# Kernel optimization log

Hardware: AMD Instinct MI355X
Metric: run time of the kernel (lower is better)

The kernel has to match this reference:

```python
import jax, jax.numpy as jnp
import numpy as np

MODEL_DIMS = 2048
BATCH, SEQ = 4, 4096
NFREQ = MODEL_DIMS // 2 + 1  # rfft spectrum length


def setup_inputs() -> dict:
    key = jax.random.key(0)
    k1, k2, k3, k4 = jax.random.split(key, 4)
    x = jax.random.normal(k1, (BATCH, SEQ, MODEL_DIMS), dtype=jnp.float32)
    queries = jax.random.normal(k2, (1, 1, NFREQ), dtype=jnp.float32)
    keyvalues = jax.random.normal(k3, (1, 1, NFREQ), dtype=jnp.float32)
    # torch nn.Linear(model_dims, model_dims, bias=False): weight is [out, in]
    w_out = jax.random.normal(k4, (MODEL_DIMS, MODEL_DIMS), dtype=jnp.float32) * (MODEL_DIMS ** -0.5)
    return {"x": x, "queries": queries, "keyvalues": keyvalues, "w_out": w_out}


def reference(x, queries, keyvalues, w_out):
    # hrr.fft = rfft over feature dim -> complex64 [B, S, NFREQ]
    xhat = jnp.fft.rfft(x, axis=-1)
    q = xhat * queries            # real spectral params broadcast-multiply
    kv = xhat * keyvalues
    kv = jnp.cumsum(kv, axis=1)   # causal prefix sum over sequence
    qv = q * kv
    values_hat = jnp.fft.irfft(qv, n=x.shape[-1], axis=-1)  # back to real [B, S, D]
    # torch Linear: y = x @ W^T
    return jnp.einsum('bsd,ed->bse', values_hat, w_out)
```

## Files before the change

kernel.cpp:

```cpp
#include <hip/hip_runtime.h>
#include <hip/hip_bf16.h>
#include <stdint.h>

#define BATCH 4
#define SEQ   4096
#define DIM   2048
#define NFREQ 1025
#define NCPLX 1024
#define ROWS  (BATCH*SEQ)

#define SCH  16
#define NSC  (SEQ/SCH)
#define NSCG 16
#define NGRP (NSC/NSCG)

#define SPEC_STRIDE 257

typedef __bf16 bf16x8 __attribute__((ext_vector_type(8)));
typedef float  f32x4  __attribute__((ext_vector_type(4)));

__device__ __forceinline__ int drev4(int n) {
  return ((n&3)<<8) | (((n>>2)&3)<<6) | (((n>>4)&3)<<4) | (((n>>6)&3)<<2) | ((n>>8)&3);
}
#define ZI(i) ((i) + ((i)>>4))

__device__ __forceinline__ float2 cmulf(float2 a, float2 b) {
  return make_float2(a.x*b.x - a.y*b.y, a.x*b.y + a.y*b.x);
}

__device__ __forceinline__ unsigned short f2bf(float f) {
  union { float f; unsigned u; } v; v.f = f;
  unsigned r = v.u + 0x7fffu + ((v.u >> 16) & 1u);
  return (unsigned short)(r >> 16);
}
__device__ __forceinline__ unsigned packbf(float2 v) {
  return (unsigned)f2bf(v.x) | ((unsigned)f2bf(v.y) << 16);
}
__device__ __forceinline__ float2 unpackbf(unsigned u) {
  union { unsigned u; float f; } a, b;
  a.u = u << 16; b.u = u & 0xffff0000u;
  return make_float2(a.f, b.f);
}

template<int INV>
__device__ __forceinline__ void bfly4(float2* z, int i0, int q,
                                      float2 w1, float2 w2, float2 w3) {
  float2 x0 = z[ZI(i0)];
  float2 x1 = cmulf(z[ZI(i0+q)],   w1);
  float2 x2 = cmulf(z[ZI(i0+2*q)], w2);
  float2 x3 = cmulf(z[ZI(i0+3*q)], w3);
  float2 a = make_float2(x0.x+x2.x, x0.y+x2.y), b = make_float2(x0.x-x2.x, x0.y-x2.y);
  float2 c = make_float2(x1.x+x3.x, x1.y+x3.y), d = make_float2(x1.x-x3.x, x1.y-x3.y);
  z[ZI(i0)]     = make_float2(a.x+c.x, a.y+c.y);
  z[ZI(i0+2*q)] = make_float2(a.x-c.x, a.y-c.y);
  if (!INV) { z[ZI(i0+q)]   = make_float2(b.x+d.y, b.y-d.x);
              z[ZI(i0+3*q)] = make_float2(b.x-d.y, b.y+d.x); }
  else      { z[ZI(i0+q)]   = make_float2(b.x-d.y, b.y+d.x);
              z[ZI(i0+3*q)] = make_float2(b.x+d.y, b.y-d.x); }
}
template<int INV>
__device__ __forceinline__ void bfly4_nw(float2* z, int i0) {
  float2 x0=z[ZI(i0)], x1=z[ZI(i0+1)], x2=z[ZI(i0+2)], x3=z[ZI(i0+3)];
  float2 a = make_float2(x0.x+x2.x, x0.y+x2.y), b = make_float2(x0.x-x2.x, x0.y-x2.y);
  float2 c = make_float2(x1.x+x3.x, x1.y+x3.y), d = make_float2(x1.x-x3.x, x1.y-x3.y);
  z[ZI(i0)]   = make_float2(a.x+c.x, a.y+c.y);
  z[ZI(i0+2)] = make_float2(a.x-c.x, a.y-c.y);
  if (!INV) { z[ZI(i0+1)] = make_float2(b.x+d.y, b.y-d.x);
              z[ZI(i0+3)] = make_float2(b.x-d.y, b.y+d.x); }
  else      { z[ZI(i0+1)] = make_float2(b.x-d.y, b.y+d.x);
              z[ZI(i0+3)] = make_float2(b.x+d.y, b.y-d.x); }
}

template<int INV>
__device__ __forceinline__ void fft_stages_tw2(float2* z0, float2* z1, int tid,
                                               const float2* tw1) {
  { int b4 = tid*4;
    bfly4_nw<INV>(z0, b4);
    bfly4_nw<INV>(z1, b4);
  }
  __syncthreads();
#pragma unroll
  for (int s = 0; s < 4; ++s) {
    const int lq = 2 + 2*s;
    const int q  = 1 << lq;
    int j = tid & (q-1), g = tid >> lq;
    int base = (g << (lq+2)) + j;
    float2 w1 = tw1[s]; if (INV) w1.y = -w1.y;
    float2 w2 = cmulf(w1, w1), w3 = cmulf(w2, w1);
    bfly4<INV>(z0, base, q, w1, w2, w3);
    bfly4<INV>(z1, base, q, w1, w2, w3);
    __syncthreads();
  }
}

__device__ __forceinline__ void make_tw1(int tid, float2* tw1) {
#pragma unroll
  for (int s = 0; s < 4; ++s) {
    const int lq = 2 + 2*s;
    const int q  = 1 << lq;
    int j = tid & (q-1);
    float ang = -6.2831853071795864769f * (float)j / (float)(4*q);
    float sw, cw; __sincosf(ang, &sw, &cw);
    tw1[s] = make_float2(cw, sw);
  }
}

__device__ __forceinline__ void unpack_row(const float2* z, int tid,
    float cwA, float swA, float cwB, float swB,
    float2& vA, float2& vAp, float2& vB, float2& vBp) {
  float2 ZkA = z[ZI(tid)],     ZnA = z[ZI((NCPLX - tid) & (NCPLX-1))];
  float2 ZkB = z[ZI(tid+256)], ZnB = z[ZI(768 - tid)];
  float Er = 0.5f*(ZkA.x + ZnA.x), Ei = 0.5f*(ZkA.y - ZnA.y);
  float dr = 0.5f*(ZkA.x - ZnA.x), di = 0.5f*(ZkA.y + ZnA.y);
  vA  = make_float2( Er + cwA*di + swA*dr,  Ei + swA*di - cwA*dr);
  vAp = make_float2( Er - cwA*di - swA*dr, -Ei + swA*di - cwA*dr);
  float Fr = 0.5f*(ZkB.x + ZnB.x), Fi = 0.5f*(ZkB.y - ZnB.y);
  float er = 0.5f*(ZkB.x - ZnB.x), ei = 0.5f*(ZkB.y + ZnB.y);
  vB  = make_float2( Fr + cwB*ei + swB*er,  Fi + swB*ei - cwB*er);
  vBp = make_float2( Fr - cwB*ei - swB*er, -Fi + swB*ei - cwB*er);
}

__global__ __launch_bounds__(256) void fwd_wfft(const float* __restrict__ x,
                                                const float* __restrict__ w,
                                                const float* __restrict__ kvs,
                                                uint4* __restrict__ spec,
                                                float2* __restrict__ partial,
                                                unsigned short* __restrict__ H) {
  __shared__ float2 z0[ZI(1023)+2], z1[ZI(1023)+2];
  __shared__ __align__(16) unsigned short hrow[2][2048];
  const int tid = threadIdx.x;

  float2 tw1[4];
  make_tw1(tid, tw1);
  const int kA = tid, kB = tid + 256;
  float swA, cwA, swB, cwB;
  __sincosf(-3.14159265358979323846f * (float)kA / 1024.0f, &swA, &cwA);
  __sincosf(-3.14159265358979323846f * (float)kB / 1024.0f, &swB, &cwB);
  int id0 = ZI(drev4(2*tid)),     id1 = ZI(drev4(2*tid+1));
  int id2 = ZI(drev4(2*tid+512)), id3 = ZI(drev4(2*tid+513));

  if (blockIdx.x >= BATCH*NSC) {
    const int e0 = (blockIdx.x - BATCH*NSC) * 2;
    const float* wr0 = w + (size_t)e0 * DIM;
    const float* wr1 = wr0 + DIM;
    float4 a0 = ((const float4*)wr0)[tid], a1 = ((const float4*)wr0)[tid + 256];
    float4 b0 = ((const float4*)wr1)[tid], b1 = ((const float4*)wr1)[tid + 256];
    z0[id0] = make_float2(a0.x, a0.y); z0[id1] = make_float2(a0.z, a0.w);
    z0[id2] = make_float2(a1.x, a1.y); z0[id3] = make_float2(a1.z, a1.w);
    z1[id0] = make_float2(b0.x, b0.y); z1[id1] = make_float2(b0.z, b0.w);
    z1[id2] = make_float2(b1.x, b1.y); z1[id3] = make_float2(b1.z, b1.w);
    __syncthreads();
    fft_stages_tw2<0>(z0, z1, tid, tw1);
    const float invN = 1.0f/2048.0f, twoN = 2.0f/2048.0f;
    float aA = (tid == 0) ? invN : twoN;
#pragma unroll
    for (int r = 0; r < 2; ++r) {
      const float2* z = r ? z1 : z0;
      float2 vA, vAp, vB, vBp;
      unpack_row(z, tid, cwA, swA, cwB, swB, vA, vAp, vB, vBp);
      unsigned short* hr = hrow[r];
      hr[tid]        = f2bf(aA   * vA.x);
      hr[1024 - tid] = f2bf(aA   * vAp.x);
      hr[256 + tid]  = f2bf(twoN * vB.x);
      hr[768 - tid]  = f2bf(twoN * vBp.x);
      if (tid) {
        hr[1024 + tid] = f2bf(twoN * vA.y);
        hr[2048 - tid] = f2bf(twoN * vAp.y);
      }
      hr[1280 + tid] = f2bf(twoN * vB.y);
      hr[1792 - tid] = f2bf(twoN * vBp.y);
      if (tid == 0) {
        float2 Z5 = z[ZI(512)];
        hr[512]  = f2bf(twoN * Z5.x);
        hr[1536] = f2bf(twoN * (-Z5.y));
      }
    }
    __syncthreads();
    ((uint4*)(H + (size_t)e0 * DIM))[tid]       = ((const uint4*)hrow[0])[tid];
    ((uint4*)(H + (size_t)(e0 + 1) * DIM))[tid] = ((const uint4*)hrow[1])[tid];
    return;
  }

  const int sc = blockIdx.x & (NSC-1), b = blockIdx.x >> 8;
  float2 sA={0,0}, sAp={0,0}, sB={0,0}, sBp={0,0}, s5={0,0};
  const size_t row0 = (size_t)b*SEQ + (size_t)sc*SCH;
  const float* xrow = x + row0*DIM;
  const float kvA = kvs[kA], kvAp = kvs[NCPLX - kA], kvB = kvs[kB], kvBp = kvs[768 - tid];

  for (int s = 0; s < SCH; s += 2) {
    const float* xr0 = xrow + (size_t)s*DIM;
    const float* xr1 = xr0 + DIM;
    float4 a0 = ((const float4*)xr0)[tid], a1 = ((const float4*)xr0)[tid + 256];
    float4 b0 = ((const float4*)xr1)[tid], b1 = ((const float4*)xr1)[tid + 256];
    z0[id0] = make_float2(a0.x, a0.y); z0[id1] = make_float2(a0.z, a0.w);
    z0[id2] = make_float2(a1.x, a1.y); z0[id3] = make_float2(a1.z, a1.w);
    z1[id0] = make_float2(b0.x, b0.y); z1[id1] = make_float2(b0.z, b0.w);
    z1[id2] = make_float2(b1.x, b1.y); z1[id3] = make_float2(b1.z, b1.w);
    __syncthreads();
    fft_stages_tw2<0>(z0, z1, tid, tw1);
#pragma unroll
    for (int r = 0; r < 2; ++r) {
      const float2* z = r ? z1 : z0;
      float2 vA, vAp, vB, vBp;
      unpack_row(z, tid, cwA, swA, cwB, swB, vA, vAp, vB, vBp);
      sA.x += vA.x;  sA.y += vA.y;   sAp.x += vAp.x; sAp.y += vAp.y;
      sB.x += vB.x;  sB.y += vB.y;   sBp.x += vBp.x; sBp.y += vBp.y;
      uint4* sprow = spec + (row0 + s + r) * SPEC_STRIDE;
      sprow[tid] = make_uint4(packbf(vA), packbf(vAp), packbf(vB), packbf(vBp));
      if (tid == 0) {
        float2 Z5 = z[ZI(512)];
        float2 v5 = make_float2(Z5.x, -Z5.y);
        s5.x += v5.x; s5.y += v5.y;
        ((unsigned*)(sprow + 256))[0] = packbf(v5);
      }
    }
    __syncthreads();
  }
  float2* pp = partial + ((size_t)(b*NSC + sc)) * NFREQ;
  pp[kA]          = make_float2(kvA*sA.x,  kvA*sA.y);
  pp[NCPLX - kA]  = make_float2(kvAp*sAp.x, kvAp*sAp.y);
  pp[kB]          = make_float2(kvB*sB.x,  kvB*sB.y);
  pp[768 - tid]   = make_float2(kvBp*sBp.x, kvBp*sBp.y);
  if (tid == 0) { float kv5 = kvs[512]; pp[512] = make_float2(kv5*s5.x, kv5*s5.y); }
}

__global__ __launch_bounds__(256) void scanA(float2* __restrict__ partial,
                                             float2* __restrict__ gtot) {
  int kc = blockIdx.x % 5, g = (blockIdx.x / 5) % NGRP, b = blockIdx.x / (5*NGRP);
  int k = kc*256 + threadIdx.x;
  if (k >= NFREQ) return;
  float2* p = partial + ((size_t)(b*NSC + g*NSCG)) * NFREQ + k;
  float2 run = {0.f, 0.f};
#pragma unroll
  for (int i = 0; i < NSCG; ++i) {
    float2 t = p[(size_t)i*NFREQ];
    p[(size_t)i*NFREQ] = run;
    run.x += t.x; run.y += t.y;
  }
  gtot[((size_t)(b*NGRP + g)) * NFREQ + k] = run;
}

__global__ __launch_bounds__(256) void inv_fused(const uint4* __restrict__ spec,
                                                 const float* __restrict__ kvs,
                                                 const float* __restrict__ qs_,
                                                 const float2* __restrict__ partial,
                                                 const float2* __restrict__ gtot,
                                                 unsigned short* __restrict__ G) {
  __shared__ __align__(16) unsigned short grow[2][2048];
  const int tid = threadIdx.x;
  const int sc = blockIdx.x & (NSC-1), b = blockIdx.x >> 8;
  const int kA = tid, kB = tid + 256;

  float ksA = kvs[kA], ksAp = kvs[NCPLX - kA], ksB = kvs[kB], ksBp = kvs[768 - tid];
  float qsA = qs_[kA], qsAp = qs_[NCPLX - kA], qsB = qs_[kB], qsBp = qs_[768 - tid];

  const float2* pp = partial + ((size_t)(b*NSC + sc)) * NFREQ;
  float2 CA  = pp[kA], CAp = pp[NCPLX-kA], CB = pp[kB], CBp = pp[768-tid];
  float ks5 = kvs[512], qs5 = qs_[512];
  float2 C5 = pp[512];
  {
    const int g = sc >> 4;
    const float2* gb = gtot + (size_t)b*NGRP*NFREQ;
    for (int gg = 0; gg < g; ++gg) {
      const float2* gr = gb + (size_t)gg*NFREQ;
      float2 a0 = gr[kA], a1 = gr[NCPLX-kA], a2 = gr[kB], a3 = gr[768-tid];
      CA.x += a0.x; CA.y += a0.y;   CAp.x += a1.x; CAp.y += a1.y;
      CB.x += a2.x; CB.y += a2.y;   CBp.x += a3.x; CBp.y += a3.y;
      if (tid == 0) { float2 a5 = gr[512]; C5.x += a5.x; C5.y += a5.y; }
    }
  }

  const size_t row0 = (size_t)b*SEQ + (size_t)sc*SCH;
  const uint4* sprow = spec + row0 * SPEC_STRIDE;
  uint4 sp = sprow[tid];
  unsigned spN = ((const unsigned*)(sprow + 256))[0];

  for (int s = 0; s < SCH; ++s) {
    uint4 spn; unsigned spNn;
    if (s+1 < SCH) {
      const uint4* nr = sprow + (size_t)(s+1) * SPEC_STRIDE;
      spn = nr[tid]; spNn = ((const unsigned*)(nr + 256))[0];
    }
    unsigned short* gw = grow[s & 1];
    float2 vA = unpackbf(sp.x), vAp = unpackbf(sp.y);
    float2 vB = unpackbf(sp.z), vBp = unpackbf(sp.w);
    CA.x  += vA.x*ksA;   CA.y  += vA.y*ksA;
    CAp.x += vAp.x*ksAp; CAp.y += vAp.y*ksAp;
    CB.x  += vB.x*ksB;   CB.y  += vB.y*ksB;
    CBp.x += vBp.x*ksBp; CBp.y += vBp.y*ksBp;
    float2 qvA  = make_float2(qsA *(vA.x*CA.x  - vA.y*CA.y),  qsA *(vA.x*CA.y  + vA.y*CA.x));
    float2 qvAp = make_float2(qsAp*(vAp.x*CAp.x- vAp.y*CAp.y),qsAp*(vAp.x*CAp.y+ vAp.y*CAp.x));
    float2 qvB  = make_float2(qsB *(vB.x*CB.x  - vB.y*CB.y),  qsB *(vB.x*CB.y  + vB.y*CB.x));
    float2 qvBp = make_float2(qsBp*(vBp.x*CBp.x- vBp.y*CBp.y),qsBp*(vBp.x*CBp.y+ vBp.y*CBp.x));
    gw[tid]        = f2bf(qvA.x);
    gw[1024 - tid] = f2bf(qvAp.x);
    gw[256 + tid]  = f2bf(qvB.x);
    gw[768 - tid]  = f2bf(qvBp.x);
    if (tid) {
      gw[1024 + tid] = f2bf(qvA.y);
      gw[2048 - tid] = f2bf(qvAp.y);
    }
    gw[1280 + tid] = f2bf(qvB.y);
    gw[1792 - tid] = f2bf(qvBp.y);
    if (tid == 0) {
      float2 v5 = unpackbf(spN);
      C5.x += v5.x*ks5; C5.y += v5.y*ks5;
      gw[512]  = f2bf(qs5*(v5.x*C5.x - v5.y*C5.y));
      gw[1536] = f2bf(qs5*(v5.x*C5.y + v5.y*C5.x));
    }
    __syncthreads();
    ((uint4*)(G + (row0 + s) * DIM))[tid] = ((const uint4*)gw)[tid];
    sp = spn; spN = spNn;
  }
}

#define NKT (DIM/64)
#define NIT (NKT/2)

#define BAR()  __builtin_amdgcn_s_barrier()
#define VMW(N) do{ asm volatile("s_waitcnt vmcnt(" #N ")" ::: "memory"); __builtin_amdgcn_sched_barrier(0); }while(0)

#define LOADA(B_, MH) do{ _Pragma("unroll") for (int m_=0;m_<4;++m_) _Pragma("unroll") for (int kk_=0;kk_<2;++kk_){ \
    int rA_ = wm*64 + m_*16 + l15; \
    aF[m_][kk_] = *(const bf16x8*)(smem + ((B_)*2+(MH))*16384 + rA_*128 + ((kk_*64 + lhi*16) ^ ((rA_&7)<<4))); } }while(0)

#define LOADB(DST, B_, NH) do{ _Pragma("unroll") for (int n_=0;n_<2;++n_) _Pragma("unroll") for (int kk_=0;kk_<2;++kk_){ \
    int rB_ = wn*32 + n_*16 + l15; \
    DST[n_][kk_] = *(const bf16x8*)(smem + 65536 + ((B_)*2+(NH))*16384 + rB_*128 + ((kk_*64 + lhi*16) ^ ((rB_&7)<<4))); } }while(0)

#define MM(MH, NH, BF) do{ __builtin_amdgcn_s_setprio(1); \
    _Pragma("unroll") for (int kk_=0;kk_<2;++kk_) _Pragma("unroll") for (int m_=0;m_<4;++m_) _Pragma("unroll") for (int n_=0;n_<2;++n_) \
      acc[MH][NH][m_][n_] = __builtin_amdgcn_mfma_f32_16x16x32_bf16(aF[m_][kk_], BF[n_][kk_], acc[MH][NH][m_][n_], 0, 0, 0); \
    __builtin_amdgcn_s_setprio(0); }while(0)

#define STAGEH(REG, B_, H_, GP, ROW0, KT) do{ _Pragma("unroll") for (int c_=0;c_<2;++c_){ \
    int ci_ = c_*512 + tid; int r_ = ci_>>3, sl_ = ci_&7; \
    const unsigned short* sp_ = (GP) + (size_t)((ROW0) + (H_)*128 + r_)*DIM + (KT) + ((sl_ ^ (r_&7))*8); \
    __builtin_amdgcn_global_load_lds((const __attribute__((address_space(1))) void*)sp_, \
      (__attribute__((address_space(3))) void*)(smem + (REG) + ((B_)*2+(H_))*16384 + ci_*16), 16, 0, 0); } }while(0)

__global__ __launch_bounds__(512, 2) void gemm256(const unsigned short* __restrict__ A,
                                                  const unsigned short* __restrict__ B,
                                                  float* __restrict__ C) {
  __shared__ __align__(16) char smem[131072];
  const int tid = threadIdx.x;
  const int lane = tid & 63;
  const int wid  = tid >> 6;
  const int wm = wid >> 2, wn = wid & 3;
  const int l15 = lane & 15, lhi = lane >> 4;

  const int xj = blockIdx.x & 7, tt = blockIdx.x >> 3;
  const int bm = xj * 8 + (tt >> 3), bn = tt & 7;
  const int m0 = bm * 256, n0 = bn * 256;

  f32x4 acc[2][2][4][2] = {};
  bf16x8 aF[4][2], bF0[2][2], bF1[2][2];

  STAGEH(0,     0,0, A, m0, 0);  STAGEH(65536, 0,0, B, n0, 0);
  STAGEH(65536, 0,1, B, n0, 0);  STAGEH(0,     0,1, A, m0, 0);
  STAGEH(0,     1,0, A, m0, 64); STAGEH(65536, 1,0, B, n0, 64);
  STAGEH(65536, 1,1, B, n0, 64); STAGEH(0,     1,1, A, m0, 64);
  VMW(8);
  BAR();

#pragma unroll 1
  for (int j = 0; j < NIT-1; ++j) {
    const int kA = (2*j+2)*64, kB = (2*j+3)*64;
    LOADA(0,0); LOADB(bF0, 0,0);
    BAR(); MM(0,0,bF0); BAR();
    LOADB(bF1, 0,1);
    STAGEH(0, 0,0, A, m0, kA); STAGEH(65536, 0,0, B, n0, kA);
    BAR(); MM(0,1,bF1); BAR();
    LOADA(0,1);
    STAGEH(65536, 0,1, B, n0, kA);
    BAR(); MM(1,0,bF0); BAR();
    STAGEH(0, 0,1, A, m0, kA);
    VMW(8);
    BAR(); MM(1,1,bF1); BAR();
    LOADA(1,0); LOADB(bF0, 1,0);
    BAR(); MM(0,0,bF0); BAR();
    LOADB(bF1, 1,1);
    STAGEH(0, 1,0, A, m0, kB); STAGEH(65536, 1,0, B, n0, kB);
    BAR(); MM(0,1,bF1); BAR();
    LOADA(1,1);
    STAGEH(65536, 1,1, B, n0, kB);
    BAR(); MM(1,0,bF0); BAR();
    STAGEH(0, 1,1, A, m0, kB);
    VMW(8);
    BAR(); MM(1,1,bF1); BAR();
  }
  LOADA(0,0); LOADB(bF0, 0,0);
  BAR(); MM(0,0,bF0); BAR();
  LOADB(bF1, 0,1);
  BAR(); MM(0,1,bF1); BAR();
  LOADA(0,1);
  BAR(); MM(1,0,bF0); BAR();
  VMW(0);
  BAR(); MM(1,1,bF1); BAR();
  LOADA(1,0); LOADB(bF0, 1,0);
  BAR(); MM(0,0,bF0); BAR();
  LOADB(bF1, 1,1);
  BAR(); MM(0,1,bF1); BAR();
  LOADA(1,1);
  BAR(); MM(1,0,bF0); BAR();
  BAR(); MM(1,1,bF1); BAR();

  const int crow = lhi * 4;
#pragma unroll
  for (int mh = 0; mh < 2; ++mh)
#pragma unroll
    for (int nh = 0; nh < 2; ++nh)
#pragma unroll
      for (int m_ = 0; m_ < 4; ++m_)
#pragma unroll
        for (int n_ = 0; n_ < 2; ++n_) {
          float* cp = C + (size_t)(m0 + mh*128 + wm*64 + m_*16 + crow) * DIM
                        + (n0 + nh*128 + wn*32 + n_*16 + l15);
#pragma unroll
          for (int j2 = 0; j2 < 4; ++j2)
            cp[(size_t)j2 * DIM] = acc[mh][nh][m_][n_][j2];
        }
}

extern "C" void kernel_launch(void* const* d_in, const int* in_sizes, int n_in,
                              void* d_out, int out_size, void* d_ws, size_t ws_size,
                              hipStream_t stream) {
  const float* x    = (const float*)d_in[0];
  const float* qry  = (const float*)d_in[1];
  const float* kvs  = (const float*)d_in[2];
  const float* wout = (const float*)d_in[3];
  float* out = (float*)d_out;

  char* ws = (char*)d_ws;
  size_t off = 0;
  uint4* spec = (uint4*)(ws + off);
  off += (size_t)ROWS * SPEC_STRIDE * sizeof(uint4);
  off = (off + 255) & ~(size_t)255;
  unsigned short* G = (unsigned short*)(ws + off);
  off += (size_t)ROWS * DIM * sizeof(unsigned short);
  off = (off + 255) & ~(size_t)255;
  unsigned short* H = (unsigned short*)(ws + off);
  off += (size_t)DIM * DIM * sizeof(unsigned short);
  off = (off + 255) & ~(size_t)255;
  float2* partial = (float2*)(ws + off);
  off += (size_t)BATCH * NSC * NFREQ * sizeof(float2);
  off = (off + 255) & ~(size_t)255;
  float2* gtot = (float2*)(ws + off);
  off += (size_t)BATCH * NGRP * NFREQ * sizeof(float2);

  hipLaunchKernelGGL(fwd_wfft,  dim3(BATCH*NSC + DIM/2), dim3(256), 0, stream, x, wout, kvs, spec, partial, H);
  hipLaunchKernelGGL(scanA,     dim3(BATCH*NGRP*5),      dim3(256), 0, stream, partial, gtot);
  hipLaunchKernelGGL(inv_fused, dim3(BATCH*NSC),         dim3(256), 0, stream, spec, kvs, qry, partial, gtot, G);
  hipLaunchKernelGGL(gemm256,   dim3((ROWS/256)*(DIM/256)), dim3(512), 0, stream, G, H, out);
}
```

Before: 255.4 us.

## Interleave two FFT rows into float4 LDS and prefetch next input rows

The two rows transformed together are now stored interleaved in one float4 shared array, so each butterfly does one 128-bit LDS access instead of two 64-bit ones, and the H staging buffer reuses that same array. The forward loop also software-prefetches the next pair of x rows into registers while the current pair is being transformed, hiding global load latency. In exchange the kernel holds more registers per thread and the float4 LDS accesses may hit different bank-conflict patterns.

```diff
diff --git a/kernel.cpp b/kernel.cpp
--- a/kernel.cpp
+++ b/kernel.cpp
@@ -27,6 +27,16 @@
 __device__ __forceinline__ float2 cmulf(float2 a, float2 b) {
   return make_float2(a.x*b.x - a.y*b.y, a.x*b.y + a.y*b.x);
 }
+__device__ __forceinline__ float4 cmul2(float4 v, float2 w) {
+  return make_float4(v.x*w.x - v.y*w.y, v.x*w.y + v.y*w.x,
+                     v.z*w.x - v.w*w.y, v.z*w.y + v.w*w.x);
+}
+__device__ __forceinline__ float4 f4add(float4 a, float4 b){
+  return make_float4(a.x+b.x, a.y+b.y, a.z+b.z, a.w+b.w);
+}
+__device__ __forceinline__ float4 f4sub(float4 a, float4 b){
+  return make_float4(a.x-b.x, a.y-b.y, a.z-b.z, a.w-b.w);
+}
 
 __device__ __forceinline__ unsigned short f2bf(float f) {
   union { float f; unsigned u; } v; v.f = f;
@@ -43,41 +53,43 @@
 }
 
 template<int INV>
-__device__ __forceinline__ void bfly4(float2* z, int i0, int q,
-                                      float2 w1, float2 w2, float2 w3) {
-  float2 x0 = z[ZI(i0)];
-  float2 x1 = cmulf(z[ZI(i0+q)],   w1);
-  float2 x2 = cmulf(z[ZI(i0+2*q)], w2);
-  float2 x3 = cmulf(z[ZI(i0+3*q)], w3);
-  float2 a = make_float2(x0.x+x2.x, x0.y+x2.y), b = make_float2(x0.x-x2.x, x0.y-x2.y);
-  float2 c = make_float2(x1.x+x3.x, x1.y+x3.y), d = make_float2(x1.x-x3.x, x1.y-x3.y);
-  z[ZI(i0)]     = make_float2(a.x+c.x, a.y+c.y);
-  z[ZI(i0+2*q)] = make_float2(a.x-c.x, a.y-c.y);
-  if (!INV) { z[ZI(i0+q)]   = make_float2(b.x+d.y, b.y-d.x);
-              z[ZI(i0+3*q)] = make_float2(b.x-d.y, b.y+d.x); }
-  else      { z[ZI(i0+q)]   = make_float2(b.x-d.y, b.y+d.x);
-              z[ZI(i0+3*q)] = make_float2(b.x+d.y, b.y-d.x); }
+__device__ __forceinline__ void bfly4d(float4* zz, int i0, int q,
+                                       float2 w1, float2 w2, float2 w3) {
+  float4 x0 = zz[ZI(i0)];
+  float4 x1 = cmul2(zz[ZI(i0+q)],   w1);
+  float4 x2 = cmul2(zz[ZI(i0+2*q)], w2);
+  float4 x3 = cmul2(zz[ZI(i0+3*q)], w3);
+  float4 a = f4add(x0, x2), b = f4sub(x0, x2);
+  float4 c = f4add(x1, x3), d = f4sub(x1, x3);
+  zz[ZI(i0)]     = f4add(a, c);
+  zz[ZI(i0+2*q)] = f4sub(a, c);
+  if (!INV) {
+    zz[ZI(i0+q)]   = make_float4(b.x+d.y, b.y-d.x, b.z+d.w, b.w-d.z);
+    zz[ZI(i0+3*q)] = make_float4(b.x-d.y, b.y+d.x, b.z-d.w, b.w+d.z);
+  } else {
+    zz[ZI(i0+q)]   = make_float4(b.x-d.y, b.y+d.x, b.z-d.w, b.w+d.z);
+    zz[ZI(i0+3*q)] = make_float4(b.x+d.y, b.y-d.x, b.z+d.w, b.w-d.z);
+  }
 }
 template<int INV>
-__device__ __forceinline__ void bfly4_nw(float2* z, int i0) {
-  float2 x0=z[ZI(i0)], x1=z[ZI(i0+1)], x2=z[ZI(i0+2)], x3=z[ZI(i0+3)];
-  float2 a = make_float2(x0.x+x2.x, x0.y+x2.y), b = make_float2(x0.x-x2.x, x0.y-x2.y);
-  float2 c = make_float2(x1.x+x3.x, x1.y+x3.y), d = make_float2(x1.x-x3.x, x1.y-x3.y);
-  z[ZI(i0)]   = make_float2(a.x+c.x, a.y+c.y);
-  z[ZI(i0+2)] = make_float2(a.x-c.x, a.y-c.y);
-  if (!INV) { z[ZI(i0+1)] = make_float2(b.x+d.y, b.y-d.x);
-              z[ZI(i0+3)] = make_float2(b.x-d.y, b.y+d.x); }
-  else      { z[ZI(i0+1)] = make_float2(b.x-d.y, b.y+d.x);
-              z[ZI(i0+3)] = make_float2(b.x+d.y, b.y-d.x); }
+__device__ __forceinline__ void bfly4d_nw(float4* zz, int i0) {
+  float4 x0=zz[ZI(i0)], x1=zz[ZI(i0+1)], x2=zz[ZI(i0+2)], x3=zz[ZI(i0+3)];
+  float4 a = f4add(x0, x2), b = f4sub(x0, x2);
+  float4 c = f4add(x1, x3), d = f4sub(x1, x3);
+  zz[ZI(i0)]   = f4add(a, c);
+  zz[ZI(i0+2)] = f4sub(a, c);
+  if (!INV) {
+    zz[ZI(i0+1)] = make_float4(b.x+d.y, b.y-d.x, b.z+d.w, b.w-d.z);
+    zz[ZI(i0+3)] = make_float4(b.x-d.y, b.y+d.x, b.z-d.w, b.w+d.z);
+  } else {
+    zz[ZI(i0+1)] = make_float4(b.x-d.y, b.y+d.x, b.z-d.w, b.w+d.z);
+    zz[ZI(i0+3)] = make_float4(b.x+d.y, b.y-d.x, b.z+d.w, b.w-d.z);
+  }
 }
 
 template<int INV>
-__device__ __forceinline__ void fft_stages_tw2(float2* z0, float2* z1, int tid,
-                                               const float2* tw1) {
-  { int b4 = tid*4;
-    bfly4_nw<INV>(z0, b4);
-    bfly4_nw<INV>(z1, b4);
-  }
+__device__ __forceinline__ void fftd(float4* zz, int tid, const float2* tw1) {
+  bfly4d_nw<INV>(zz, tid*4);
   __syncthreads();
 #pragma unroll
   for (int s = 0; s < 4; ++s) {
@@ -87,8 +99,7 @@
     int base = (g << (lq+2)) + j;
     float2 w1 = tw1[s]; if (INV) w1.y = -w1.y;
     float2 w2 = cmulf(w1, w1), w3 = cmulf(w2, w1);
-    bfly4<INV>(z0, base, q, w1, w2, w3);
-    bfly4<INV>(z1, base, q, w1, w2, w3);
+    bfly4d<INV>(zz, base, q, w1, w2, w3);
     __syncthreads();
   }
 }
@@ -105,19 +116,32 @@
   }
 }
 
-__device__ __forceinline__ void unpack_row(const float2* z, int tid,
+__device__ __forceinline__ void unpack_row2(const float4* zz, int tid,
     float cwA, float swA, float cwB, float swB,
-    float2& vA, float2& vAp, float2& vB, float2& vBp) {
-  float2 ZkA = z[ZI(tid)],     ZnA = z[ZI((NCPLX - tid) & (NCPLX-1))];
-  float2 ZkB = z[ZI(tid+256)], ZnB = z[ZI(768 - tid)];
-  float Er = 0.5f*(ZkA.x + ZnA.x), Ei = 0.5f*(ZkA.y - ZnA.y);
-  float dr = 0.5f*(ZkA.x - ZnA.x), di = 0.5f*(ZkA.y + ZnA.y);
-  vA  = make_float2( Er + cwA*di + swA*dr,  Ei + swA*di - cwA*dr);
-  vAp = make_float2( Er - cwA*di - swA*dr, -Ei + swA*di - cwA*dr);
-  float Fr = 0.5f*(ZkB.x + ZnB.x), Fi = 0.5f*(ZkB.y - ZnB.y);
-  float er = 0.5f*(ZkB.x - ZnB.x), ei = 0.5f*(ZkB.y + ZnB.y);
-  vB  = make_float2( Fr + cwB*ei + swB*er,  Fi + swB*ei - cwB*er);
-  vBp = make_float2( Fr - cwB*ei - swB*er, -Fi + swB*ei - cwB*er);
+    float2& vA, float2& vAp, float2& vB, float2& vBp,
+    float2& uA, float2& uAp, float2& uB, float2& uBp) {
+  float4 ZkA = zz[ZI(tid)],     ZnA = zz[ZI((NCPLX - tid) & (NCPLX-1))];
+  float4 ZkB = zz[ZI(tid+256)], ZnB = zz[ZI(768 - tid)];
+  {
+    float Er = 0.5f*(ZkA.x + ZnA.x), Ei = 0.5f*(ZkA.y - ZnA.y);
+    float dr = 0.5f*(ZkA.x - ZnA.x), di = 0.5f*(ZkA.y + ZnA.y);
+    vA  = make_float2( Er + cwA*di + swA*dr,  Ei + swA*di - cwA*dr);
+    vAp = make_float2( Er - cwA*di - swA*dr, -Ei + swA*di - cwA*dr);
+    float Fr = 0.5f*(ZkB.x + ZnB.x), Fi = 0.5f*(ZkB.y - ZnB.y);
+    float er = 0.5f*(ZkB.x - ZnB.x), ei = 0.5f*(ZkB.y + ZnB.y);
+    vB  = make_float2( Fr + cwB*ei + swB*er,  Fi + swB*ei - cwB*er);
+    vBp = make_float2( Fr - cwB*ei - swB*er, -Fi + swB*ei - cwB*er);
+  }
+  {
+    float Er = 0.5f*(ZkA.z + ZnA.z), Ei = 0.5f*(ZkA.w - ZnA.w);
+    float dr = 0.5f*(ZkA.z - ZnA.z), di = 0.5f*(ZkA.w + ZnA.w);
+    uA  = make_float2( Er + cwA*di + swA*dr,  Ei + swA*di - cwA*dr);
+    uAp = make_float2( Er - cwA*di - swA*dr, -Ei + swA*di - cwA*dr);
+    float Fr = 0.5f*(ZkB.z + ZnB.z), Fi = 0.5f*(ZkB.w - ZnB.w);
+    float er = 0.5f*(ZkB.z - ZnB.z), ei = 0.5f*(ZkB.w + ZnB.w);
+    uB  = make_float2( Fr + cwB*ei + swB*er,  Fi + swB*ei - cwB*er);
+    uBp = make_float2( Fr - cwB*ei - swB*er, -Fi + swB*ei - cwB*er);
+  }
 }
 
 __global__ __launch_bounds__(256) void fwd_wfft(const float* __restrict__ x,
@@ -126,8 +150,7 @@
                                                 uint4* __restrict__ spec,
                                                 float2* __restrict__ partial,
                                                 unsigned short* __restrict__ H) {
-  __shared__ float2 z0[ZI(1023)+2], z1[ZI(1023)+2];
-  __shared__ __align__(16) unsigned short hrow[2][2048];
+  __shared__ __align__(16) float4 zz[ZI(1023)+2];
   const int tid = threadIdx.x;
 
   float2 tw1[4];
@@ -145,39 +168,38 @@
     const float* wr1 = wr0 + DIM;
     float4 a0 = ((const float4*)wr0)[tid], a1 = ((const float4*)wr0)[tid + 256];
     float4 b0 = ((const float4*)wr1)[tid], b1 = ((const float4*)wr1)[tid + 256];
-    z0[id0] = make_float2(a0.x, a0.y); z0[id1] = make_float2(a0.z, a0.w);
-    z0[id2] = make_float2(a1.x, a1.y); z0[id3] = make_float2(a1.z, a1.w);
-    z1[id0] = make_float2(b0.x, b0.y); z1[id1] = make_float2(b0.z, b0.w);
-    z1[id2] = make_float2(b1.x, b1.y); z1[id3] = make_float2(b1.z, b1.w);
-    __syncthreads();
-    fft_stages_tw2<0>(z0, z1, tid, tw1);
+    zz[id0] = make_float4(a0.x, a0.y, b0.x, b0.y);
+    zz[id1] = make_float4(a0.z, a0.w, b0.z, b0.w);
+    zz[id2] = make_float4(a1.x, a1.y, b1.x, b1.y);
+    zz[id3] = make_float4(a1.z, a1.w, b1.z, b1.w);
+    __syncthreads();
+    fftd<0>(zz, tid, tw1);
+    float2 vA, vAp, vB, vBp, uA, uAp, uB, uBp;
+    unpack_row2(zz, tid, cwA, swA, cwB, swB, vA, vAp, vB, vBp, uA, uAp, uB, uBp);
+    float4 Z5 = make_float4(0,0,0,0);
+    if (tid == 0) Z5 = zz[ZI(512)];
+    __syncthreads();
+    unsigned short* hr0 = (unsigned short*)zz;
+    unsigned short* hr1 = hr0 + 2048;
     const float invN = 1.0f/2048.0f, twoN = 2.0f/2048.0f;
     float aA = (tid == 0) ? invN : twoN;
-#pragma unroll
-    for (int r = 0; r < 2; ++r) {
-      const float2* z = r ? z1 : z0;
-      float2 vA, vAp, vB, vBp;
-      unpack_row(z, tid, cwA, swA, cwB, swB, vA, vAp, vB, vBp);
-      unsigned short* hr = hrow[r];
-      hr[tid]        = f2bf(aA   * vA.x);
-      hr[1024 - tid] = f2bf(aA   * vAp.x);
-      hr[256 + tid]  = f2bf(twoN * vB.x);
-      hr[768 - tid]  = f2bf(twoN * vBp.x);
-      if (tid) {
-        hr[1024 + tid] = f2bf(twoN * vA.y);
-        hr[2048 - tid] = f2bf(twoN * vAp.y);
-      }
-      hr[1280 + tid] = f2bf(twoN * vB.y);
-      hr[1792 - tid] = f2bf(twoN * vBp.y);
-      if (tid == 0) {
-        float2 Z5 = z[ZI(512)];
-        hr[512]  = f2bf(twoN * Z5.x);
-        hr[1536] = f2bf(twoN * (-Z5.y));
-      }
-    }
-    __syncthreads();
-    ((uint4*)(H + (size_t)e0 * DIM))[tid]       = ((const uint4*)hrow[0])[tid];
-    ((uint4*)(H + (size_t)(e0 + 1) * DIM))[tid] = ((const uint4*)hrow[1])[tid];
+    hr0[tid]        = f2bf(aA   * vA.x);   hr1[tid]        = f2bf(aA   * uA.x);
+    hr0[1024 - tid] = f2bf(aA   * vAp.x);  hr1[1024 - tid] = f2bf(aA   * uAp.x);
+    hr0[256 + tid]  = f2bf(twoN * vB.x);   hr1[256 + tid]  = f2bf(twoN * uB.x);
+    hr0[768 - tid]  = f2bf(twoN * vBp.x);  hr1[768 - tid]  = f2bf(twoN * uBp.x);
+    if (tid) {
+      hr0[1024 + tid] = f2bf(twoN * vA.y);  hr1[1024 + tid] = f2bf(twoN * uA.y);
+      hr0[2048 - tid] = f2bf(twoN * vAp.y); hr1[2048 - tid] = f2bf(twoN * uAp.y);
+    }
+    hr0[1280 + tid] = f2bf(twoN * vB.y);   hr1[1280 + tid] = f2bf(twoN * uB.y);
+    hr0[1792 - tid] = f2bf(twoN * vBp.y);  hr1[1792 - tid] = f2bf(twoN * uBp.y);
+    if (tid == 0) {
+      hr0[512]  = f2bf(twoN * Z5.x);  hr0[1536] = f2bf(twoN * (-Z5.y));
+      hr1[512]  = f2bf(twoN * Z5.z);  hr1[1536] = f2bf(twoN * (-Z5.w));
+    }
+    __syncthreads();
+    ((uint4*)(H + (size_t)e0 * DIM))[tid]       = ((const uint4*)hr0)[tid];
+    ((uint4*)(H + (size_t)(e0 + 1) * DIM))[tid] = ((const uint4*)hr1)[tid];
     return;
   }
 
@@ -187,34 +209,43 @@
   const float* xrow = x + row0*DIM;
   const float kvA = kvs[kA], kvAp = kvs[NCPLX - kA], kvB = kvs[kB], kvBp = kvs[768 - tid];
 
+  float4 c0 = ((const float4*)xrow)[tid],         c1 = ((const float4*)xrow)[tid + 256];
+  float4 d0 = ((const float4*)(xrow+DIM))[tid],   d1 = ((const float4*)(xrow+DIM))[tid + 256];
+
   for (int s = 0; s < SCH; s += 2) {
-    const float* xr0 = xrow + (size_t)s*DIM;
-    const float* xr1 = xr0 + DIM;
-    float4 a0 = ((const float4*)xr0)[tid], a1 = ((const float4*)xr0)[tid + 256];
-    float4 b0 = ((const float4*)xr1)[tid], b1 = ((const float4*)xr1)[tid + 256];
-    z0[id0] = make_float2(a0.x, a0.y); z0[id1] = make_float2(a0.z, a0.w);
-    z0[id2] = make_float2(a1.x, a1.y); z0[id3] = make_float2(a1.z, a1.w);
-    z1[id0] = make_float2(b0.x, b0.y); z1[id1] = make_float2(b0.z, b0.w);
-    z1[id2] = make_float2(b1.x, b1.y); z1[id3] = make_float2(b1.z, b1.w);
-    __syncthreads();
-    fft_stages_tw2<0>(z0, z1, tid, tw1);
-#pragma unroll
-    for (int r = 0; r < 2; ++r) {
-      const float2* z = r ? z1 : z0;
-      float2 vA, vAp, vB, vBp;
-      unpack_row(z, tid, cwA, swA, cwB, swB, vA, vAp, vB, vBp);
-      sA.x += vA.x;  sA.y += vA.y;   sAp.x += vAp.x; sAp.y += vAp.y;
-      sB.x += vB.x;  sB.y += vB.y;   sBp.x += vBp.x; sBp.y += vBp.y;
-      uint4* sprow = spec + (row0 + s + r) * SPEC_STRIDE;
-      sprow[tid] = make_uint4(packbf(vA), packbf(vAp), packbf(vB), packbf(vBp));
-      if (tid == 0) {
-        float2 Z5 = z[ZI(512)];
-        float2 v5 = make_float2(Z5.x, -Z5.y);
-        s5.x += v5.x; s5.y += v5.y;
-        ((unsigned*)(sprow + 256))[0] = packbf(v5);
-      }
-    }
-    __syncthreads();
+    float4 n0, n1, n2, n3;
+    if (s+2 < SCH) {
+      const float* nx0 = xrow + (size_t)(s+2)*DIM;
+      const float* nx1 = nx0 + DIM;
+      n0 = ((const float4*)nx0)[tid]; n1 = ((const float4*)nx0)[tid + 256];
+      n2 = ((const float4*)nx1)[tid]; n3 = ((const float4*)nx1)[tid + 256];
+    }
+    zz[id0] = make_float4(c0.x, c0.y, d0.x, d0.y);
+    zz[id1] = make_float4(c0.z, c0.w, d0.z, d0.w);
+    zz[id2] = make_float4(c1.x, c1.y, d1.x, d1.y);
+    zz[id3] = make_float4(c1.z, c1.w, d1.z, d1.w);
+    __syncthreads();
+    fftd<0>(zz, tid, tw1);
+    float2 vA, vAp, vB, vBp, uA, uAp, uB, uBp;
+    unpack_row2(zz, tid, cwA, swA, cwB, swB, vA, vAp, vB, vBp, uA, uAp, uB, uBp);
+    sA.x += vA.x;  sA.y += vA.y;   sAp.x += vAp.x; sAp.y += vAp.y;
+    sB.x += vB.x;  sB.y += vB.y;   sBp.x += vBp.x; sBp.y += vBp.y;
+    sA.x += uA.x;  sA.y += uA.y;   sAp.x += uAp.x; sAp.y += uAp.y;
+    sB.x += uB.x;  sB.y += uB.y;   sBp.x += uBp.x; sBp.y += uBp.y;
+    uint4* sp0 = spec + (row0 + s) * SPEC_STRIDE;
+    uint4* sp1 = sp0 + SPEC_STRIDE;
+    sp0[tid] = make_uint4(packbf(vA), packbf(vAp), packbf(vB), packbf(vBp));
+    sp1[tid] = make_uint4(packbf(uA), packbf(uAp), packbf(uB), packbf(uBp));
+    if (tid == 0) {
+      float4 Z5 = zz[ZI(512)];
+      float2 v5 = make_float2(Z5.x, -Z5.y);
+      float2 u5 = make_float2(Z5.z, -Z5.w);
+      s5.x += v5.x + u5.x; s5.y += v5.y + u5.y;
+      ((unsigned*)(sp0 + 256))[0] = packbf(v5);
+      ((unsigned*)(sp1 + 256))[0] = packbf(u5);
+    }
+    __syncthreads();
+    c0 = n0; c1 = n1; d0 = n2; d1 = n3;
   }
   float2* pp = partial + ((size_t)(b*NSC + sc)) * NFREQ;
   pp[kA]          = make_float2(kvA*sA.x,  kvA*sA.y);
```

Result: faster. 219.2 us (median of 2 runs) (-14.2%).
